# Kernel optimization log

Measured on AMD Instinct MI355X. Metric: run time of the kernel, lower is better.

## Reference

```python
import jax, jax.numpy as jnp
import numpy as np

N = 100000      # nodes
E = 1200000     # edges
H = 64          # hidden_channels
L = 8           # num_layers
G = 100         # graphs in batch
ALPHA = 0.1
THETA = 0.5
EPS = 1e-5      # BatchNorm1d eps


def setup_inputs() -> dict:
    key = jax.random.key(0)
    ks = jax.random.split(key, 12)
    s = 0.05
    pos = jax.random.normal(ks[0], (N, 3), dtype=jnp.float32)
    edge_index = jax.random.randint(ks[1], (2, E), 0, N, dtype=jnp.int32)
    batch = jnp.sort(jax.random.randint(ks[2], (N,), 0, G, dtype=jnp.int32))
    return {
        "pos": pos,
        "edge_index": edge_index,
        "batch": batch,
        "lin0_w": jax.random.normal(ks[3], (3, H), dtype=jnp.float32) * s,
        "lin0_b": jnp.zeros((H,), jnp.float32),
        "conv_w": jax.random.normal(ks[4], (L, H, H), dtype=jnp.float32) * s,
        "lin1_w": jax.random.normal(ks[5], (H, H), dtype=jnp.float32) * s,
        "lin1_b": jnp.zeros((H,), jnp.float32),
        "mlp1_w": jax.random.normal(ks[6], (H, H), dtype=jnp.float32) * s,
        "mlp1_b": jnp.zeros((H,), jnp.float32),
        "bn1_g": jnp.ones((H,), jnp.float32),
        "bn1_b": jnp.zeros((H,), jnp.float32),
        "mlp2_w": jax.random.normal(ks[7], (H, H), dtype=jnp.float32) * s,
        "mlp2_b": jnp.zeros((H,), jnp.float32),
        "bn2_g": jnp.ones((H,), jnp.float32),
        "bn2_b": jnp.zeros((H,), jnp.float32),
        "out_w": jax.random.normal(ks[8], (H, 10), dtype=jnp.float32) * s,
        "out_b": jnp.zeros((10,), jnp.float32),
    }


def _bn(z, g, b):
    # BatchNorm1d, training-mode batch statistics
    mu = z.mean(axis=0)
    var = z.var(axis=0)
    return g * (z - mu) * jax.lax.rsqrt(var + EPS) + b


def reference(pos, edge_index, batch, lin0_w, lin0_b, conv_w, lin1_w, lin1_b,
              mlp1_w, mlp1_b, bn1_g, bn1_b, mlp2_w, mlp2_b, bn2_g, bn2_b,
              out_w, out_b):
    src, dst = edge_index[0], edge_index[1]
    x = jax.nn.relu(pos @ lin0_w + lin0_b)   # [N, H]
    x0 = x
    for l in range(L):
        beta = float(np.log(THETA / (l + 1) + 1.0))
        # GCN2Conv (normalize=False, shared_weights=True):
        # sum-aggregate neighbors, initial residual, identity mapping
        agg = jax.ops.segment_sum(x[src], dst, num_segments=N)   # [N, H]
        h = (1.0 - ALPHA) * agg + ALPHA * x0
        x = jax.nn.relu((1.0 - beta) * h + beta * (h @ conv_w[l]))
    x = x @ lin1_w + lin1_b
    pooled = jax.ops.segment_max(x, batch, num_segments=G)       # [G, H]
    pooled = jnp.where(jnp.isfinite(pooled), pooled, 0.0)        # guard empty segments
    h1 = jax.nn.relu(_bn(pooled @ mlp1_w + mlp1_b, bn1_g, bn1_b))
    h2 = jax.nn.relu(_bn(h1 @ mlp2_w + mlp2_b, bn2_g, bn2_b))
    logits = h2 @ out_w + out_b                                  # [G, 10]
    return jax.nn.log_softmax(logits, axis=-1)
```

## Files before the change

### kernel.cpp

```cpp
#include <hip/hip_runtime.h>
#include <math.h>

#define NNODES 100000
#define NEDGES 1200000
#define HD 64
#define NLAYERS 8
#define NGRAPH 100
#define PPART 32
#define NPART 8
#define C8 16777216.0f

typedef _Float16 f16;
typedef __attribute__((ext_vector_type(8))) _Float16 f16x8;
typedef __attribute__((ext_vector_type(4))) float f32x4;

__global__ void lin0_k(const float* __restrict__ pos, const float* __restrict__ w,
                       const float* __restrict__ b, f16* __restrict__ x0h, int total) {
    int i = blockIdx.x * blockDim.x + threadIdx.x;
    if (i >= total) return;
    int n = i >> 6, h = i & 63;
    float p0 = pos[n * 3 + 0], p1 = pos[n * 3 + 1], p2 = pos[n * 3 + 2];
    float v = fmaf(p0, w[h], fmaf(p1, w[64 + h], fmaf(p2, w[128 + h], b[h])));
    x0h[i] = (f16)fmaxf(v, 0.0f);
}

__global__ void hist_k(const int* __restrict__ dst, int* __restrict__ degp,
                       int* __restrict__ rank, int E) {
    int e = blockIdx.x * 256 + threadIdx.x;
    int p = blockIdx.x & (NPART - 1);
    if (e < E) rank[e] = atomicAdd(&degp[p * NNODES + dst[e]], 1);
}

__global__ void offs_k(const int* __restrict__ degp, int* __restrict__ poff,
                       int* __restrict__ deg, int n) {
    int d = blockIdx.x * blockDim.x + threadIdx.x;
    if (d >= n) return;
    int s = 0;
#pragma unroll
    for (int p = 0; p < NPART; ++p) {
        poff[p * n + d] = s;
        s += degp[p * n + d];
    }
    deg[d] = s;
}

__global__ void scan_part_k(const int* __restrict__ deg, int* __restrict__ bsum, int n) {
    __shared__ int s[256];
    int t = threadIdx.x;
    int i = blockIdx.x * 256 + t;
    s[t] = (i < n) ? deg[i] : 0;
    __syncthreads();
    for (int off = 128; off > 0; off >>= 1) {
        if (t < off) s[t] += s[t + off];
        __syncthreads();
    }
    if (t == 0) bsum[blockIdx.x] = s[0];
}

__global__ void scan_mid_k(const int* __restrict__ bsum, int* __restrict__ boff,
                           int nblk, int* __restrict__ roff, int n) {
    __shared__ int s[512];
    int t = threadIdx.x;
    int v = (t < nblk) ? bsum[t] : 0;
    s[t] = v;
    __syncthreads();
    for (int off = 1; off < 512; off <<= 1) {
        int u = (t >= off) ? s[t - off] : 0;
        __syncthreads();
        s[t] += u;
        __syncthreads();
    }
    if (t < nblk) boff[t] = s[t] - v;
    if (t == nblk - 1) roff[n] = s[t];
}

__global__ void scan_final_k(const int* __restrict__ deg, const int* __restrict__ boff,
                             int* __restrict__ roff, int n) {
    __shared__ int s[256];
    int t = threadIdx.x;
    int i = blockIdx.x * 256 + t;
    int v = (i < n) ? deg[i] : 0;
    s[t] = v;
    __syncthreads();
    for (int off = 1; off < 256; off <<= 1) {
        int u = (t >= off) ? s[t - off] : 0;
        __syncthreads();
        s[t] += u;
        __syncthreads();
    }
    if (i < n) roff[i] = boff[blockIdx.x] + s[t] - v;
}

__global__ void fill_k(const int* __restrict__ src, const int* __restrict__ dst,
                       const int* __restrict__ roff, const int* __restrict__ poff,
                       const int* __restrict__ rank, int* __restrict__ csr, int E) {
    int e = blockIdx.x * 256 + threadIdx.x;
    if (e < E) {
        int d = dst[e];
        int p = (e >> 8) & (NPART - 1);
        csr[roff[d] + poff[p * NNODES + d] + rank[e]] = src[e];
    }
}

__global__ void prep_k(const float* __restrict__ cw, const float* __restrict__ l1w,
                       f16* __restrict__ Bpack) {
    int t = blockIdx.x * blockDim.x + threadIdx.x;
    if (t >= 9 * 4 * 2 * 64) return;
    int mat = t >> 9, rem = t & 511;
    int ct = rem >> 7, kk = (rem >> 6) & 1, lane = rem & 63;
    int g = lane >> 4, r = lane & 15;
    f16* outp = Bpack + (size_t)t * 8;
    if (mat < 8) {
        float beta = logf(0.5f / (float)(mat + 1) + 1.0f);
        const float* W = cw + (size_t)mat * 4096;
        for (int j = 0; j < 8; ++j) {
            int row = 32 * kk + 8 * g + j;
            int col = 16 * ct + r;
            float m = beta * W[row * 64 + col];
            if (row == col) m += 1.0f - beta;
            outp[j] = (f16)(0.125f * m);
        }
    } else {
        for (int j = 0; j < 8; ++j) {
            int row = 32 * kk + 8 * g + j;
            int col = 16 * ct + r;
            outp[j] = (f16)l1w[row * 64 + col];
        }
    }
}

__global__ __launch_bounds__(256, 8) void layer_k(
    const f16* __restrict__ xin, f16* __restrict__ xout,
    const f16* __restrict__ x0, const f16* __restrict__ Bp,
    const int* __restrict__ roff, const int* __restrict__ csr,
    float x0scale, int nblocks) {
    __shared__ __align__(16) f16 Htile[16][72];
    const int tid   = threadIdx.x;
    const int lane  = tid & 63;
    const int wslot = tid >> 6;
    const f16x8 b0 = *(const f16x8*)(Bp + (size_t)((wslot * 2 + 0) * 64 + lane) * 8);
    const f16x8 b1 = *(const f16x8*)(Bp + (size_t)((wslot * 2 + 1) * 64 + lane) * 8);
    for (int tile = blockIdx.x; tile < NNODES / 16; tile += nblocks) {
        const int nbase = tile << 4;
#pragma unroll 1
        for (int i = 0; i < 4; ++i) {
            const int n = nbase + (wslot << 2) + i;
            const int beg = roff[n], end = roff[n + 1];
            float x0v = (float)x0[(n << 6) + lane];
            float s0 = 0.0f, s1 = 0.0f, s2 = 0.0f, s3 = 0.0f;
            int e = beg;
            for (; e + 8 <= end; e += 8) {
                int e0 = csr[e + 0], e1 = csr[e + 1], e2 = csr[e + 2], e3 = csr[e + 3];
                int e4 = csr[e + 4], e5 = csr[e + 5], e6 = csr[e + 6], e7 = csr[e + 7];
                f16 a0 = xin[(e0 << 6) + lane];
                f16 a1 = xin[(e1 << 6) + lane];
                f16 a2 = xin[(e2 << 6) + lane];
                f16 a3 = xin[(e3 << 6) + lane];
                f16 a4 = xin[(e4 << 6) + lane];
                f16 a5 = xin[(e5 << 6) + lane];
                f16 a6 = xin[(e6 << 6) + lane];
                f16 a7 = xin[(e7 << 6) + lane];
                s0 += (float)a0; s1 += (float)a1; s2 += (float)a2; s3 += (float)a3;
                s0 += (float)a4; s1 += (float)a5; s2 += (float)a6; s3 += (float)a7;
            }
            for (; e + 4 <= end; e += 4) {
                int e0 = csr[e + 0], e1 = csr[e + 1], e2 = csr[e + 2], e3 = csr[e + 3];
                s0 += (float)xin[(e0 << 6) + lane];
                s1 += (float)xin[(e1 << 6) + lane];
                s2 += (float)xin[(e2 << 6) + lane];
                s3 += (float)xin[(e3 << 6) + lane];
            }
            for (; e < end; ++e) s0 += (float)xin[(csr[e] << 6) + lane];
            float h = fmaf(0.9f, (s0 + s1) + (s2 + s3), x0scale * x0v);
            Htile[(wslot << 2) + i][lane] = (f16)h;
        }
        __syncthreads();
        const int ar = lane & 15, ag = lane >> 4;
        f16x8 a0 = *(const f16x8*)&Htile[ar][(ag << 3) + 0];
        f16x8 a1 = *(const f16x8*)&Htile[ar][(ag << 3) + 32];
        f32x4 acc = {0.0f, 0.0f, 0.0f, 0.0f};
        acc = __builtin_amdgcn_mfma_f32_16x16x32_f16(a0, b0, acc, 0, 0, 0);
        acc = __builtin_amdgcn_mfma_f32_16x16x32_f16(a1, b1, acc, 0, 0, 0);
        const int col = (wslot << 4) + ar;
        const int rbase = nbase + (ag << 2);
#pragma unroll
        for (int j = 0; j < 4; ++j) {
            xout[((rbase + j) << 6) + col] = (f16)fmaxf(acc[j], 0.0f);
        }
        __syncthreads();
    }
}

__global__ __launch_bounds__(256, 8) void lin1_k(
    const f16* __restrict__ xin, f16* __restrict__ yout,
    const f16* __restrict__ Bp, int nblocks) {
    const int lane  = threadIdx.x & 63;
    const int wslot = threadIdx.x >> 6;
    const f16x8 b0 = *(const f16x8*)(Bp + (size_t)((wslot * 2 + 0) * 64 + lane) * 8);
    const f16x8 b1 = *(const f16x8*)(Bp + (size_t)((wslot * 2 + 1) * 64 + lane) * 8);
    const int ar = lane & 15, ag = lane >> 4;
    for (int tile = blockIdx.x; tile < NNODES / 16; tile += nblocks) {
        const int nbase = tile << 4;
        f16x8 a0 = *(const f16x8*)(xin + ((size_t)(nbase + ar) << 6) + (ag << 3));
        f16x8 a1 = *(const f16x8*)(xin + ((size_t)(nbase + ar) << 6) + (ag << 3) + 32);
        f32x4 acc = {0.0f, 0.0f, 0.0f, 0.0f};
        acc = __builtin_amdgcn_mfma_f32_16x16x32_f16(a0, b0, acc, 0, 0, 0);
        acc = __builtin_amdgcn_mfma_f32_16x16x32_f16(a1, b1, acc, 0, 0, 0);
        const int col = (wslot << 4) + ar;
        const int rbase = nbase + (ag << 2);
#pragma unroll
        for (int j = 0; j < 4; ++j) {
            yout[((rbase + j) << 6) + col] = (f16)acc[j];
        }
    }
}

__device__ __forceinline__ int lbound(const int* __restrict__ a, int n, int v) {
    int lo = 0, hi = n;
    while (lo < hi) { int mid = (lo + hi) >> 1; if (a[mid] < v) lo = mid + 1; else hi = mid; }
    return lo;
}

__global__ __launch_bounds__(256, 8) void segmax_k(
    const f16* __restrict__ y, const int* __restrict__ batch,
    float* __restrict__ pmax) {
    __shared__ float wm[4][64];
    const int tid   = threadIdx.x;
    const int lane  = tid & 63;
    const int wslot = tid >> 6;
    const int g = blockIdx.x / PPART, part = blockIdx.x % PPART;
    const int lo = lbound(batch, NNODES, g);
    const int hi = lbound(batch, NNODES, g + 1);
    const int cnt = hi - lo;
    const int qlo = lo + (cnt * part) / PPART;
    const int qhi = lo + (cnt * (part + 1)) / PPART;
    float vmax = -INFINITY;
    for (int n = qlo + wslot; n < qhi; n += 4)
        vmax = fmaxf(vmax, (float)y[(n << 6) + lane]);
    wm[wslot][lane] = vmax;
    __syncthreads();
    if (tid < 64) {
        float m = fmaxf(fmaxf(wm[0][tid], wm[1][tid]), fmaxf(wm[2][tid], wm[3][tid]));
        pmax[blockIdx.x * 64 + tid] = m;
    }
}

__global__ void poolcomb_k(const float* __restrict__ pmax,
                           const float* __restrict__ bvec,
                           float* __restrict__ pooled) {
    int i = blockIdx.x * blockDim.x + threadIdx.x;
    if (i >= NGRAPH * 64) return;
    int g = i >> 6, lane = i & 63;
    float m = -INFINITY;
    for (int p = 0; p < PPART; ++p)
        m = fmaxf(m, pmax[(PPART * g + p) * 64 + lane]);
    pooled[i] = fmaf(C8, m, bvec[lane]);
}

__global__ __launch_bounds__(256) void head_k(
    const float* __restrict__ pooled,
    const float* __restrict__ m1w, const float* __restrict__ m1b,
    const float* __restrict__ g1, const float* __restrict__ be1,
    const float* __restrict__ m2w, const float* __restrict__ m2b,
    const float* __restrict__ g2, const float* __restrict__ be2,
    const float* __restrict__ ow, const float* __restrict__ ob,
    float* __restrict__ out) {
    __shared__ float A[NGRAPH * 64];
    __shared__ float B[NGRAPH * 64];
    __shared__ float mu[64], rs[64];
    __shared__ float LG[NGRAPH * 10];
    int t = threadIdx.x;
    for (int i = t; i < NGRAPH * 64; i += 256) {
        float f = pooled[i];
        if (!isfinite(f)) f = 0.0f;
        A[i] = f;
    }
    __syncthreads();
    for (int i = t; i < NGRAPH * 64; i += 256) {
        int g = i >> 6, j = i & 63;
        float acc = m1b[j];
        for (int k = 0; k < 64; ++k) acc = fmaf(A[(g << 6) + k], m1w[k * 64 + j], acc);
        B[i] = acc;
    }
    __syncthreads();
    if (t < 64) {
        float sm = 0.0f, sq = 0.0f;
        for (int g = 0; g < NGRAPH; ++g) { float z = B[g * 64 + t]; sm += z; sq += z * z; }
        float m = sm * (1.0f / NGRAPH);
        float var = sq * (1.0f / NGRAPH) - m * m;
        mu[t] = m; rs[t] = rsqrtf(var + 1e-5f);
    }
    __syncthreads();
    for (int i = t; i < NGRAPH * 64; i += 256) {
        int j = i & 63;
        float z = fmaf((B[i] - mu[j]) * rs[j], g1[j], be1[j]);
        A[i] = fmaxf(z, 0.0f);
    }
    __syncthreads();
    for (int i = t; i < NGRAPH * 64; i += 256) {
        int g = i >> 6, j = i & 63;
        float acc = m2b[j];
        for (int k = 0; k < 64; ++k) acc = fmaf(A[(g << 6) + k], m2w[k * 64 + j], acc);
        B[i] = acc;
    }
    __syncthreads();
    if (t < 64) {
        float sm = 0.0f, sq = 0.0f;
        for (int g = 0; g < NGRAPH; ++g) { float z = B[g * 64 + t]; sm += z; sq += z * z; }
        float m = sm * (1.0f / NGRAPH);
        float var = sq * (1.0f / NGRAPH) - m * m;
        mu[t] = m; rs[t] = rsqrtf(var + 1e-5f);
    }
    __syncthreads();
    for (int i = t; i < NGRAPH * 64; i += 256) {
        int j = i & 63;
        float z = fmaf((B[i] - mu[j]) * rs[j], g2[j], be2[j]);
        A[i] = fmaxf(z, 0.0f);
    }
    __syncthreads();
    for (int i = t; i < NGRAPH * 10; i += 256) {
        int g = i / 10, j = i - g * 10;
        float acc = ob[j];
        for (int k = 0; k < 64; ++k) acc = fmaf(A[(g << 6) + k], ow[k * 10 + j], acc);
        LG[i] = acc;
    }
    __syncthreads();
    if (t < NGRAPH) {
        float m = -1e30f;
        for (int j = 0; j < 10; ++j) m = fmaxf(m, LG[t * 10 + j]);
        float s = 0.0f;
        for (int j = 0; j < 10; ++j) s += expf(LG[t * 10 + j] - m);
        float lse = m + logf(s);
        for (int j = 0; j < 10; ++j) out[t * 10 + j] = LG[t * 10 + j] - lse;
    }
}

extern "C" void kernel_launch(void* const* d_in, const int* in_sizes, int n_in,
                              void* d_out, int out_size, void* d_ws, size_t ws_size,
                              hipStream_t stream) {
    const float* pos   = (const float*)d_in[0];
    const int*   eidx  = (const int*)d_in[1];
    const int*   batch = (const int*)d_in[2];
    const float* l0w   = (const float*)d_in[3];
    const float* l0b   = (const float*)d_in[4];
    const float* cw    = (const float*)d_in[5];
    const float* l1w   = (const float*)d_in[6];
    const float* l1b   = (const float*)d_in[7];
    const float* m1w   = (const float*)d_in[8];
    const float* m1b   = (const float*)d_in[9];
    const float* g1    = (const float*)d_in[10];
    const float* b1    = (const float*)d_in[11];
    const float* m2w   = (const float*)d_in[12];
    const float* m2b   = (const float*)d_in[13];
    const float* g2    = (const float*)d_in[14];
    const float* b2    = (const float*)d_in[15];
    const float* ow    = (const float*)d_in[16];
    const float* ob    = (const float*)d_in[17];
    float* out = (float*)d_out;
    const int* src = eidx;
    const int* dst = eidx + NEDGES;

    size_t off = 0;
    auto alloc = [&](size_t bytes) -> void* {
        void* p = (char*)d_ws + off;
        off += (bytes + 255) & ~(size_t)255;
        return p;
    };
    f16*   x0h    = (f16*)alloc((size_t)NNODES * 64 * 2);
    f16*   xA     = (f16*)alloc((size_t)NNODES * 64 * 2);
    f16*   xB     = (f16*)alloc((size_t)NNODES * 64 * 2);
    int*   deg    = (int*)alloc((size_t)NNODES * 4);
    int*   degp   = (int*)alloc((size_t)NPART * NNODES * 4);
    int*   poff   = (int*)alloc((size_t)NPART * NNODES * 4);
    int*   roff   = (int*)alloc((size_t)(NNODES + 1) * 4);
    const int NBLK = (NNODES + 255) / 256;
    int*   bsum   = (int*)alloc((size_t)NBLK * 4);
    int*   boff   = (int*)alloc((size_t)NBLK * 4);
    int*   csr    = (int*)alloc((size_t)NEDGES * 4);
    float* pooled = (float*)alloc((size_t)NGRAPH * 64 * 4);
    float* pmax   = (float*)alloc((size_t)NGRAPH * PPART * 64 * 4);
    f16*   Bpack  = (f16*)alloc((size_t)9 * 4 * 2 * 64 * 8 * 2);
    int*   rank   = (int*)xB;

    hipMemsetAsync(degp, 0, (size_t)NPART * NNODES * 4, stream);
    {
        int total = NNODES * 64;
        lin0_k<<<(total + 255) / 256, 256, 0, stream>>>(pos, l0w, l0b, x0h, total);
    }
    hist_k<<<(NEDGES + 255) / 256, 256, 0, stream>>>(dst, degp, rank, NEDGES);
    offs_k<<<NBLK, 256, 0, stream>>>(degp, poff, deg, NNODES);
    scan_part_k<<<NBLK, 256, 0, stream>>>(deg, bsum, NNODES);
    scan_mid_k<<<1, 512, 0, stream>>>(bsum, boff, NBLK, roff, NNODES);
    scan_final_k<<<NBLK, 256, 0, stream>>>(deg, boff, roff, NNODES);
    fill_k<<<(NEDGES + 255) / 256, 256, 0, stream>>>(src, dst, roff, poff, rank, csr, NEDGES);
    prep_k<<<(9 * 4 * 2 * 64 + 255) / 256, 256, 0, stream>>>(cw, l1w, Bpack);

    const int LBLOCKS = 2048;
    const f16* cur = x0h;
    for (int l = 0; l < NLAYERS; ++l) {
        float x0scale = (float)(0.1 * ldexp(1.0, -3 * l));
        f16* nxt = (l & 1) ? xB : xA;
        layer_k<<<LBLOCKS, 256, 0, stream>>>(cur, nxt, x0h,
                                             Bpack + (size_t)l * 4 * 2 * 64 * 8,
                                             roff, csr, x0scale, LBLOCKS);
        cur = nxt;
    }
    f16* l1out = (cur == xA) ? xB : xA;
    lin1_k<<<LBLOCKS, 256, 0, stream>>>(cur, l1out,
                                        Bpack + (size_t)8 * 4 * 2 * 64 * 8, LBLOCKS);
    segmax_k<<<NGRAPH * PPART, 256, 0, stream>>>(l1out, batch, pmax);
    poolcomb_k<<<(NGRAPH * 64 + 255) / 256, 256, 0, stream>>>(pmax, l1b, pooled);
    head_k<<<1, 256, 0, stream>>>(pooled, m1w, m1b, g1, b1, m2w, m2b, g2, b2, ow, ob, out);
}
```

Measured before the change: 547.3 us.

## Balance edge gathers across waves with shared-memory atomic segment accumulation

The layer kernel now splits a 16-node tile's combined edge range evenly across its four waves instead of giving each wave four whole nodes. Partial sums are flushed with LDS float atomics into a per-tile accumulator when a wave crosses a node boundary. The persistent grid-stride loop is replaced with one block per tile. This is meant to remove load imbalance from varying node degrees, at the cost of LDS atomics, an extra zeroing pass, extra barriers and a single accumulator chain per wave instead of four independent ones.

New measurement: 601.1 us. 9.8% more time.

```diff
diff --git a/kernel.cpp b/kernel.cpp
--- a/kernel.cpp
+++ b/kernel.cpp
@@ -133,61 +133,76 @@
     const f16* __restrict__ xin, f16* __restrict__ xout,
     const f16* __restrict__ x0, const f16* __restrict__ Bp,
     const int* __restrict__ roff, const int* __restrict__ csr,
-    float x0scale, int nblocks) {
+    float x0scale) {
+    __shared__ float hacc[16][64];
     __shared__ __align__(16) f16 Htile[16][72];
+    __shared__ int sroff[17];
     const int tid   = threadIdx.x;
     const int lane  = tid & 63;
     const int wslot = tid >> 6;
+    const int nbase = blockIdx.x << 4;
     const f16x8 b0 = *(const f16x8*)(Bp + (size_t)((wslot * 2 + 0) * 64 + lane) * 8);
     const f16x8 b1 = *(const f16x8*)(Bp + (size_t)((wslot * 2 + 1) * 64 + lane) * 8);
-    for (int tile = blockIdx.x; tile < NNODES / 16; tile += nblocks) {
-        const int nbase = tile << 4;
-#pragma unroll 1
-        for (int i = 0; i < 4; ++i) {
-            const int n = nbase + (wslot << 2) + i;
-            const int beg = roff[n], end = roff[n + 1];
-            float x0v = (float)x0[(n << 6) + lane];
-            float s0 = 0.0f, s1 = 0.0f, s2 = 0.0f, s3 = 0.0f;
-            int e = beg;
-            for (; e + 8 <= end; e += 8) {
-                int e0 = csr[e + 0], e1 = csr[e + 1], e2 = csr[e + 2], e3 = csr[e + 3];
-                int e4 = csr[e + 4], e5 = csr[e + 5], e6 = csr[e + 6], e7 = csr[e + 7];
-                f16 a0 = xin[(e0 << 6) + lane];
-                f16 a1 = xin[(e1 << 6) + lane];
-                f16 a2 = xin[(e2 << 6) + lane];
-                f16 a3 = xin[(e3 << 6) + lane];
-                f16 a4 = xin[(e4 << 6) + lane];
-                f16 a5 = xin[(e5 << 6) + lane];
-                f16 a6 = xin[(e6 << 6) + lane];
-                f16 a7 = xin[(e7 << 6) + lane];
-                s0 += (float)a0; s1 += (float)a1; s2 += (float)a2; s3 += (float)a3;
-                s0 += (float)a4; s1 += (float)a5; s2 += (float)a6; s3 += (float)a7;
-            }
-            for (; e + 4 <= end; e += 4) {
-                int e0 = csr[e + 0], e1 = csr[e + 1], e2 = csr[e + 2], e3 = csr[e + 3];
-                s0 += (float)xin[(e0 << 6) + lane];
-                s1 += (float)xin[(e1 << 6) + lane];
-                s2 += (float)xin[(e2 << 6) + lane];
-                s3 += (float)xin[(e3 << 6) + lane];
-            }
-            for (; e < end; ++e) s0 += (float)xin[(csr[e] << 6) + lane];
-            float h = fmaf(0.9f, (s0 + s1) + (s2 + s3), x0scale * x0v);
-            Htile[(wslot << 2) + i][lane] = (f16)h;
-        }
-        __syncthreads();
-        const int ar = lane & 15, ag = lane >> 4;
-        f16x8 a0 = *(const f16x8*)&Htile[ar][(ag << 3) + 0];
-        f16x8 a1 = *(const f16x8*)&Htile[ar][(ag << 3) + 32];
-        f32x4 acc = {0.0f, 0.0f, 0.0f, 0.0f};
-        acc = __builtin_amdgcn_mfma_f32_16x16x32_f16(a0, b0, acc, 0, 0, 0);
-        acc = __builtin_amdgcn_mfma_f32_16x16x32_f16(a1, b1, acc, 0, 0, 0);
-        const int col = (wslot << 4) + ar;
-        const int rbase = nbase + (ag << 2);
+    if (tid < 17) sroff[tid] = roff[nbase + tid];
+    for (int i = tid; i < 16 * 64; i += 256) ((float*)hacc)[i] = 0.0f;
+    __syncthreads();
+    const int ebeg = sroff[0], eend = sroff[16];
+    const int T = eend - ebeg;
+    int e  = ebeg + ((T * wslot) >> 2);
+    const int ee = ebeg + ((T * (wslot + 1)) >> 2);
+    int n = 0;
+    while (n < 15 && sroff[n + 1] <= e) ++n;
+    int next_end = sroff[n + 1];
+    float s = 0.0f;
+#define FLUSHADV(EK)                                                         \
+    while ((EK) >= next_end) {                                               \
+        atomicAdd(&hacc[n][lane], s);                                        \
+        s = 0.0f; ++n; next_end = sroff[n + 1];                              \
+    }
+    for (; e + 8 <= ee; e += 8) {
+        int i0 = csr[e + 0], i1 = csr[e + 1], i2 = csr[e + 2], i3 = csr[e + 3];
+        int i4 = csr[e + 4], i5 = csr[e + 5], i6 = csr[e + 6], i7 = csr[e + 7];
+        f16 v0 = xin[(i0 << 6) + lane];
+        f16 v1 = xin[(i1 << 6) + lane];
+        f16 v2 = xin[(i2 << 6) + lane];
+        f16 v3 = xin[(i3 << 6) + lane];
+        f16 v4 = xin[(i4 << 6) + lane];
+        f16 v5 = xin[(i5 << 6) + lane];
+        f16 v6 = xin[(i6 << 6) + lane];
+        f16 v7 = xin[(i7 << 6) + lane];
+        FLUSHADV(e + 0) s += (float)v0;
+        FLUSHADV(e + 1) s += (float)v1;
+        FLUSHADV(e + 2) s += (float)v2;
+        FLUSHADV(e + 3) s += (float)v3;
+        FLUSHADV(e + 4) s += (float)v4;
+        FLUSHADV(e + 5) s += (float)v5;
+        FLUSHADV(e + 6) s += (float)v6;
+        FLUSHADV(e + 7) s += (float)v7;
+    }
+    for (; e < ee; ++e) {
+        FLUSHADV(e)
+        s += (float)xin[(csr[e] << 6) + lane];
+    }
+    atomicAdd(&hacc[n][lane], s);
+#undef FLUSHADV
+    __syncthreads();
+    for (int i = tid; i < 16 * 64; i += 256) {
+        int r = i >> 6, c = i & 63;
+        float h = fmaf(0.9f, hacc[r][c], x0scale * (float)x0[((nbase + r) << 6) + c]);
+        Htile[r][c] = (f16)h;
+    }
+    __syncthreads();
+    const int ar = lane & 15, ag = lane >> 4;
+    f16x8 a0 = *(const f16x8*)&Htile[ar][(ag << 3) + 0];
+    f16x8 a1 = *(const f16x8*)&Htile[ar][(ag << 3) + 32];
+    f32x4 acc = {0.0f, 0.0f, 0.0f, 0.0f};
+    acc = __builtin_amdgcn_mfma_f32_16x16x32_f16(a0, b0, acc, 0, 0, 0);
+    acc = __builtin_amdgcn_mfma_f32_16x16x32_f16(a1, b1, acc, 0, 0, 0);
+    const int col = (wslot << 4) + ar;
+    const int rbase = nbase + (ag << 2);
 #pragma unroll
-        for (int j = 0; j < 4; ++j) {
-            xout[((rbase + j) << 6) + col] = (f16)fmaxf(acc[j], 0.0f);
-        }
-        __syncthreads();
+    for (int j = 0; j < 4; ++j) {
+        xout[((rbase + j) << 6) + col] = (f16)fmaxf(acc[j], 0.0f);
     }
 }
 
@@ -400,9 +415,9 @@
     for (int l = 0; l < NLAYERS; ++l) {
         float x0scale = (float)(0.1 * ldexp(1.0, -3 * l));
         f16* nxt = (l & 1) ? xB : xA;
-        layer_k<<<LBLOCKS, 256, 0, stream>>>(cur, nxt, x0h,
-                                             Bpack + (size_t)l * 4 * 2 * 64 * 8,
-                                             roff, csr, x0scale, LBLOCKS);
+        layer_k<<<NNODES / 16, 256, 0, stream>>>(cur, nxt, x0h,
+                                                 Bpack + (size_t)l * 4 * 2 * 64 * 8,
+                                                 roff, csr, x0scale);
         cur = nxt;
     }
     f16* l1out = (cur == xA) ? xB : xA;
```

## Give each wave its own 16-node tile to remove block-level barriers

Applied to the files above, without the earlier changes.

The GCN2 layer kernel now assigns a whole 16-node tile to a single wavefront instead of splitting it across four waves of a block. Each wave gathers all 16 rows into a private LDS slice, then runs the four column-tile MFMAs itself, reloading the packed weight fragments from global/cache in each iteration. This replaces the two __syncthreads per tile with wave-local barriers, so a slow high-degree node no longer stalls the other waves. The cost is serial gather work of 16 nodes per wave with fewer tiles in flight (6250 tiles against 8192 waves), which leaves many waves idle and may cause load imbalance, plus extra weight loads per tile.

Result: slower. 565.1 us (+3.2%).

```diff
diff --git a/kernel.cpp b/kernel.cpp
--- a/kernel.cpp
+++ b/kernel.cpp
@@ -133,61 +133,65 @@
     const f16* __restrict__ xin, f16* __restrict__ xout,
     const f16* __restrict__ x0, const f16* __restrict__ Bp,
     const int* __restrict__ roff, const int* __restrict__ csr,
-    float x0scale, int nblocks) {
-    __shared__ __align__(16) f16 Htile[16][72];
+    float x0scale, int total_waves) {
+    __shared__ __align__(16) f16 Htile[4][16][72];
     const int tid   = threadIdx.x;
     const int lane  = tid & 63;
     const int wslot = tid >> 6;
-    const f16x8 b0 = *(const f16x8*)(Bp + (size_t)((wslot * 2 + 0) * 64 + lane) * 8);
-    const f16x8 b1 = *(const f16x8*)(Bp + (size_t)((wslot * 2 + 1) * 64 + lane) * 8);
-    for (int tile = blockIdx.x; tile < NNODES / 16; tile += nblocks) {
+    const int wid0  = (blockIdx.x * blockDim.x + tid) >> 6;
+    const int ar = lane & 15, ag = lane >> 4;
+    for (int tile = wid0; tile < NNODES / 16; tile += total_waves) {
         const int nbase = tile << 4;
 #pragma unroll 1
-        for (int i = 0; i < 4; ++i) {
-            const int n = nbase + (wslot << 2) + i;
+        for (int i = 0; i < 16; ++i) {
+            const int n = nbase + i;
             const int beg = roff[n], end = roff[n + 1];
             float x0v = (float)x0[(n << 6) + lane];
             float s0 = 0.0f, s1 = 0.0f, s2 = 0.0f, s3 = 0.0f;
             int e = beg;
             for (; e + 8 <= end; e += 8) {
-                int e0 = csr[e + 0], e1 = csr[e + 1], e2 = csr[e + 2], e3 = csr[e + 3];
-                int e4 = csr[e + 4], e5 = csr[e + 5], e6 = csr[e + 6], e7 = csr[e + 7];
-                f16 a0 = xin[(e0 << 6) + lane];
-                f16 a1 = xin[(e1 << 6) + lane];
-                f16 a2 = xin[(e2 << 6) + lane];
-                f16 a3 = xin[(e3 << 6) + lane];
-                f16 a4 = xin[(e4 << 6) + lane];
-                f16 a5 = xin[(e5 << 6) + lane];
-                f16 a6 = xin[(e6 << 6) + lane];
-                f16 a7 = xin[(e7 << 6) + lane];
-                s0 += (float)a0; s1 += (float)a1; s2 += (float)a2; s3 += (float)a3;
-                s0 += (float)a4; s1 += (float)a5; s2 += (float)a6; s3 += (float)a7;
+                int i0 = csr[e + 0], i1 = csr[e + 1], i2 = csr[e + 2], i3 = csr[e + 3];
+                int i4 = csr[e + 4], i5 = csr[e + 5], i6 = csr[e + 6], i7 = csr[e + 7];
+                f16 v0 = xin[(i0 << 6) + lane];
+                f16 v1 = xin[(i1 << 6) + lane];
+                f16 v2 = xin[(i2 << 6) + lane];
+                f16 v3 = xin[(i3 << 6) + lane];
+                f16 v4 = xin[(i4 << 6) + lane];
+                f16 v5 = xin[(i5 << 6) + lane];
+                f16 v6 = xin[(i6 << 6) + lane];
+                f16 v7 = xin[(i7 << 6) + lane];
+                s0 += (float)v0; s1 += (float)v1; s2 += (float)v2; s3 += (float)v3;
+                s0 += (float)v4; s1 += (float)v5; s2 += (float)v6; s3 += (float)v7;
             }
             for (; e + 4 <= end; e += 4) {
-                int e0 = csr[e + 0], e1 = csr[e + 1], e2 = csr[e + 2], e3 = csr[e + 3];
-                s0 += (float)xin[(e0 << 6) + lane];
-                s1 += (float)xin[(e1 << 6) + lane];
-                s2 += (float)xin[(e2 << 6) + lane];
-                s3 += (float)xin[(e3 << 6) + lane];
+                int i0 = csr[e + 0], i1 = csr[e + 1], i2 = csr[e + 2], i3 = csr[e + 3];
+                s0 += (float)xin[(i0 << 6) + lane];
+                s1 += (float)xin[(i1 << 6) + lane];
+                s2 += (float)xin[(i2 << 6) + lane];
+                s3 += (float)xin[(i3 << 6) + lane];
             }
             for (; e < end; ++e) s0 += (float)xin[(csr[e] << 6) + lane];
             float h = fmaf(0.9f, (s0 + s1) + (s2 + s3), x0scale * x0v);
-            Htile[(wslot << 2) + i][lane] = (f16)h;
+            Htile[wslot][i][lane] = (f16)h;
         }
-        __syncthreads();
-        const int ar = lane & 15, ag = lane >> 4;
-        f16x8 a0 = *(const f16x8*)&Htile[ar][(ag << 3) + 0];
-        f16x8 a1 = *(const f16x8*)&Htile[ar][(ag << 3) + 32];
-        f32x4 acc = {0.0f, 0.0f, 0.0f, 0.0f};
-        acc = __builtin_amdgcn_mfma_f32_16x16x32_f16(a0, b0, acc, 0, 0, 0);
-        acc = __builtin_amdgcn_mfma_f32_16x16x32_f16(a1, b1, acc, 0, 0, 0);
-        const int col = (wslot << 4) + ar;
-        const int rbase = nbase + (ag << 2);
+        __builtin_amdgcn_wave_barrier();
+        f16x8 a0 = *(const f16x8*)&Htile[wslot][ar][(ag << 3) + 0];
+        f16x8 a1 = *(const f16x8*)&Htile[wslot][ar][(ag << 3) + 32];
+#pragma unroll 1
+        for (int ct = 0; ct < 4; ++ct) {
+            f16x8 b0 = *(const f16x8*)(Bp + (size_t)((ct * 2 + 0) * 64 + lane) * 8);
+            f16x8 b1 = *(const f16x8*)(Bp + (size_t)((ct * 2 + 1) * 64 + lane) * 8);
+            f32x4 acc = {0.0f, 0.0f, 0.0f, 0.0f};
+            acc = __builtin_amdgcn_mfma_f32_16x16x32_f16(a0, b0, acc, 0, 0, 0);
+            acc = __builtin_amdgcn_mfma_f32_16x16x32_f16(a1, b1, acc, 0, 0, 0);
+            const int col = (ct << 4) + ar;
+            const int rbase = nbase + (ag << 2);
 #pragma unroll
-        for (int j = 0; j < 4; ++j) {
-            xout[((rbase + j) << 6) + col] = (f16)fmaxf(acc[j], 0.0f);
+            for (int j = 0; j < 4; ++j) {
+                xout[((rbase + j) << 6) + col] = (f16)fmaxf(acc[j], 0.0f);
+            }
         }
-        __syncthreads();
+        __builtin_amdgcn_wave_barrier();
     }
 }
 
@@ -396,13 +400,14 @@
     prep_k<<<(9 * 4 * 2 * 64 + 255) / 256, 256, 0, stream>>>(cw, l1w, Bpack);
 
     const int LBLOCKS = 2048;
+    const int TW = LBLOCKS * 256 / 64;
     const f16* cur = x0h;
     for (int l = 0; l < NLAYERS; ++l) {
         float x0scale = (float)(0.1 * ldexp(1.0, -3 * l));
         f16* nxt = (l & 1) ? xB : xA;
         layer_k<<<LBLOCKS, 256, 0, stream>>>(cur, nxt, x0h,
                                              Bpack + (size_t)l * 4 * 2 * 64 * 8,
-                                             roff, csr, x0scale, LBLOCKS);
+                                             roff, csr, x0scale, TW);
         cur = nxt;
     }
     f16* l1out = (cur == xA) ? xB : xA;
```

## Split fused layer into separate edge-parallel aggregation and MFMA GEMM kernels

Applied to the files above, without the earlier changes.

Replaces the fused aggregate+matmul layer kernel with an aggregation kernel that processes four edges per wave in parallel over 32-channel halves with f16x2 loads and shuffle reductions, writing to an intermediate buffer, followed by a reused MFMA GEMM kernel with optional ReLU. The aim is to expose more edge-level parallelism in the gather. It adds an extra intermediate buffer round trip and an extra launch per layer, and the non-unrolled gather loop may issue fewer outstanding loads.

After: 928.5 us. +69.6%, slower.

```diff
diff --git a/kernel.cpp b/kernel.cpp
--- a/kernel.cpp
+++ b/kernel.cpp
@@ -11,6 +11,7 @@
 #define C8 16777216.0f
 
 typedef _Float16 f16;
+typedef __attribute__((ext_vector_type(2))) _Float16 f16x2;
 typedef __attribute__((ext_vector_type(8))) _Float16 f16x8;
 typedef __attribute__((ext_vector_type(4))) float f32x4;
 
@@ -129,71 +130,52 @@
     }
 }
 
-__global__ __launch_bounds__(256, 8) void layer_k(
-    const f16* __restrict__ xin, f16* __restrict__ xout,
-    const f16* __restrict__ x0, const f16* __restrict__ Bp,
+__global__ __launch_bounds__(256, 8) void agg_k(
+    const f16* __restrict__ xin, f16* __restrict__ hbuf,
+    const f16* __restrict__ x0,
     const int* __restrict__ roff, const int* __restrict__ csr,
-    float x0scale, int nblocks) {
-    __shared__ __align__(16) f16 Htile[16][72];
+    float x0scale) {
+    const int b     = blockIdx.x;
+    const int chalf = b & 1;
+    const int tile  = b >> 1;
     const int tid   = threadIdx.x;
     const int lane  = tid & 63;
     const int wslot = tid >> 6;
-    const f16x8 b0 = *(const f16x8*)(Bp + (size_t)((wslot * 2 + 0) * 64 + lane) * 8);
-    const f16x8 b1 = *(const f16x8*)(Bp + (size_t)((wslot * 2 + 1) * 64 + lane) * 8);
-    for (int tile = blockIdx.x; tile < NNODES / 16; tile += nblocks) {
-        const int nbase = tile << 4;
+    const int grp   = lane >> 4;
+    const int cl    = lane & 15;
+    const int cbase = (chalf << 5) + (cl << 1);
+    const int nbase = (tile << 4) + (wslot << 2);
 #pragma unroll 1
-        for (int i = 0; i < 4; ++i) {
-            const int n = nbase + (wslot << 2) + i;
-            const int beg = roff[n], end = roff[n + 1];
-            float x0v = (float)x0[(n << 6) + lane];
-            float s0 = 0.0f, s1 = 0.0f, s2 = 0.0f, s3 = 0.0f;
-            int e = beg;
-            for (; e + 8 <= end; e += 8) {
-                int e0 = csr[e + 0], e1 = csr[e + 1], e2 = csr[e + 2], e3 = csr[e + 3];
-                int e4 = csr[e + 4], e5 = csr[e + 5], e6 = csr[e + 6], e7 = csr[e + 7];
-                f16 a0 = xin[(e0 << 6) + lane];
-                f16 a1 = xin[(e1 << 6) + lane];
-                f16 a2 = xin[(e2 << 6) + lane];
-                f16 a3 = xin[(e3 << 6) + lane];
-                f16 a4 = xin[(e4 << 6) + lane];
-                f16 a5 = xin[(e5 << 6) + lane];
-                f16 a6 = xin[(e6 << 6) + lane];
-                f16 a7 = xin[(e7 << 6) + lane];
-                s0 += (float)a0; s1 += (float)a1; s2 += (float)a2; s3 += (float)a3;
-                s0 += (float)a4; s1 += (float)a5; s2 += (float)a6; s3 += (float)a7;
-            }
-            for (; e + 4 <= end; e += 4) {
-                int e0 = csr[e + 0], e1 = csr[e + 1], e2 = csr[e + 2], e3 = csr[e + 3];
-                s0 += (float)xin[(e0 << 6) + lane];
-                s1 += (float)xin[(e1 << 6) + lane];
-                s2 += (float)xin[(e2 << 6) + lane];
-                s3 += (float)xin[(e3 << 6) + lane];
-            }
-            for (; e < end; ++e) s0 += (float)xin[(csr[e] << 6) + lane];
-            float h = fmaf(0.9f, (s0 + s1) + (s2 + s3), x0scale * x0v);
-            Htile[(wslot << 2) + i][lane] = (f16)h;
-        }
-        __syncthreads();
-        const int ar = lane & 15, ag = lane >> 4;
-        f16x8 a0 = *(const f16x8*)&Htile[ar][(ag << 3) + 0];
-        f16x8 a1 = *(const f16x8*)&Htile[ar][(ag << 3) + 32];
-        f32x4 acc = {0.0f, 0.0f, 0.0f, 0.0f};
-        acc = __builtin_amdgcn_mfma_f32_16x16x32_f16(a0, b0, acc, 0, 0, 0);
-        acc = __builtin_amdgcn_mfma_f32_16x16x32_f16(a1, b1, acc, 0, 0, 0);
-        const int col = (wslot << 4) + ar;
-        const int rbase = nbase + (ag << 2);
-#pragma unroll
-        for (int j = 0; j < 4; ++j) {
-            xout[((rbase + j) << 6) + col] = (f16)fmaxf(acc[j], 0.0f);
-        }
-        __syncthreads();
-    }
-}
-
-__global__ __launch_bounds__(256, 8) void lin1_k(
+    for (int i = 0; i < 4; ++i) {
+        const int n = nbase + i;
+        const int beg = roff[n], end = roff[n + 1];
+        float sl = 0.0f, sh = 0.0f;
+#pragma unroll 1
+        for (int e = beg; e < end; e += 4) {
+            int ee = e + grp;
+            int idx = csr[ee < end ? ee : end - 1];
+            float m = (ee < end) ? 1.0f : 0.0f;
+            f16x2 v = *(const f16x2*)(xin + (idx << 6) + cbase);
+            sl = fmaf(m, (float)v.x, sl);
+            sh = fmaf(m, (float)v.y, sh);
+        }
+        sl += __shfl_xor(sl, 16, 64);
+        sh += __shfl_xor(sh, 16, 64);
+        sl += __shfl_xor(sl, 32, 64);
+        sh += __shfl_xor(sh, 32, 64);
+        if (grp == 0) {
+            f16x2 x0v = *(const f16x2*)(x0 + (n << 6) + cbase);
+            f16x2 hw;
+            hw.x = (f16)fmaf(0.9f, sl, x0scale * (float)x0v.x);
+            hw.y = (f16)fmaf(0.9f, sh, x0scale * (float)x0v.y);
+            *(f16x2*)(hbuf + (n << 6) + cbase) = hw;
+        }
+    }
+}
+
+__global__ __launch_bounds__(256, 8) void gemm_k(
     const f16* __restrict__ xin, f16* __restrict__ yout,
-    const f16* __restrict__ Bp, int nblocks) {
+    const f16* __restrict__ Bp, int nblocks, int doRelu) {
     const int lane  = threadIdx.x & 63;
     const int wslot = threadIdx.x >> 6;
     const f16x8 b0 = *(const f16x8*)(Bp + (size_t)((wslot * 2 + 0) * 64 + lane) * 8);
@@ -210,7 +192,8 @@
         const int rbase = nbase + (ag << 2);
 #pragma unroll
         for (int j = 0; j < 4; ++j) {
-            yout[((rbase + j) << 6) + col] = (f16)acc[j];
+            float r = doRelu ? fmaxf(acc[j], 0.0f) : acc[j];
+            yout[((rbase + j) << 6) + col] = (f16)r;
         }
     }
 }
@@ -369,6 +352,7 @@
     f16*   x0h    = (f16*)alloc((size_t)NNODES * 64 * 2);
     f16*   xA     = (f16*)alloc((size_t)NNODES * 64 * 2);
     f16*   xB     = (f16*)alloc((size_t)NNODES * 64 * 2);
+    f16*   hbuf   = (f16*)alloc((size_t)NNODES * 64 * 2);
     int*   deg    = (int*)alloc((size_t)NNODES * 4);
     int*   degp   = (int*)alloc((size_t)NPART * NNODES * 4);
     int*   poff   = (int*)alloc((size_t)NPART * NNODES * 4);
@@ -400,14 +384,15 @@
     for (int l = 0; l < NLAYERS; ++l) {
         float x0scale = (float)(0.1 * ldexp(1.0, -3 * l));
         f16* nxt = (l & 1) ? xB : xA;
-        layer_k<<<LBLOCKS, 256, 0, stream>>>(cur, nxt, x0h,
-                                             Bpack + (size_t)l * 4 * 2 * 64 * 8,
-                                             roff, csr, x0scale, LBLOCKS);
+        agg_k<<<2 * (NNODES / 16), 256, 0, stream>>>(cur, hbuf, x0h, roff, csr, x0scale);
+        gemm_k<<<LBLOCKS, 256, 0, stream>>>(hbuf, nxt,
+                                            Bpack + (size_t)l * 4 * 2 * 64 * 8,
+                                            LBLOCKS, 1);
         cur = nxt;
     }
     f16* l1out = (cur == xA) ? xB : xA;
-    lin1_k<<<LBLOCKS, 256, 0, stream>>>(cur, l1out,
-                                        Bpack + (size_t)8 * 4 * 2 * 64 * 8, LBLOCKS);
+    gemm_k<<<LBLOCKS, 256, 0, stream>>>(cur, l1out,
+                                        Bpack + (size_t)8 * 4 * 2 * 64 * 8, LBLOCKS, 0);
     segmax_k<<<NGRAPH * PPART, 256, 0, stream>>>(l1out, batch, pmax);
     poolcomb_k<<<(NGRAPH * 64 + 255) / 256, 256, 0, stream>>>(pmax, l1b, pooled);
     head_k<<<1, 256, 0, stream>>>(pooled, m1w, m1b, g1, b1, m2w, m2b, g2, b2, ow, ob, out);
```
